# Kernel optimization log

Measured on AMD Instinct MI355X. Metric: run time of the kernel, lower is better.

## Reference

```python
import jax, jax.numpy as jnp
import numpy as np

B, S, D, E, R, TOP_K = 4, 4096, 2048, 6, 16, 2


def setup_inputs() -> dict:
    key = jax.random.key(0)
    ks = jax.random.split(key, 9)
    scale = 0.02
    return {
        "x": jax.random.normal(ks[0], (B, S, D), dtype=jnp.float32),
        "W_base": jax.random.normal(ks[1], (D, D), dtype=jnp.float32) * scale,
        "b_base": jax.random.normal(ks[2], (D,), dtype=jnp.float32) * scale,
        "A_s": jax.random.normal(ks[3], (D, R), dtype=jnp.float32) * scale,   # shared expert down-proj
        "B_s": jax.random.normal(ks[4], (R, D), dtype=jnp.float32) * scale,   # shared expert up-proj
        "A_r": jax.random.normal(ks[5], (E, D, R), dtype=jnp.float32) * scale,  # routed experts down-proj
        "B_r": jax.random.normal(ks[6], (E, R, D), dtype=jnp.float32) * scale,  # routed experts up-proj
        "W_router": jax.random.normal(ks[7], (D, E), dtype=jnp.float32) * scale,
        "b_router": jax.random.normal(ks[8], (E,), dtype=jnp.float32) * scale,
    }


def reference(x, W_base, b_base, A_s, B_s, A_r, B_r, W_router, b_router):
    # base_out computed under torch.no_grad() in the original -> stop_gradient
    base_out = jax.lax.stop_gradient(jnp.einsum("bsd,df->bsf", x, W_base) + b_base)

    # single shared LoRA expert (num_shared=1)
    shared_out = jnp.einsum("bsr,rf->bsf", jnp.einsum("bsd,dr->bsr", x, A_s), B_s)

    # router: softmax over experts, then top-k gating
    gates = jax.nn.softmax(jnp.einsum("bsd,de->bse", x, W_router) + b_router, axis=-1)
    topk_w, topk_i = jax.lax.top_k(gates, TOP_K)  # [B,S,K]
    # per-expert combine weight: sum of top-k weights scattered to expert slots
    w_per_e = jnp.sum(topk_w[..., None] * jax.nn.one_hot(topk_i, E, dtype=x.dtype), axis=2)  # [B,S,E]

    # routed LoRA experts: rank-16 down-proj per expert, weight in low-rank space,
    # then up-proj -- avoids materializing the [B,S,E,D] expert outputs.
    h = jnp.einsum("bsd,edr->bser", x, A_r)          # [B,S,E,R]
    hw = h * w_per_e[..., None]                       # fold gate weights into rank dim
    routed_out = jnp.einsum("bser,erf->bsf", hw, B_r)  # [B,S,D]

    return base_out + shared_out + routed_out
```

## Files before the change

kernel.cpp:

```cpp
#include <hip/hip_runtime.h>
#include <hip/hip_bf16.h>

typedef __hip_bfloat16 bf16;
typedef __attribute__((ext_vector_type(8))) __bf16 bf16x8;
typedef __attribute__((ext_vector_type(8))) short s16x8;
typedef __attribute__((ext_vector_type(4))) float f32x4;

#define AS1 __attribute__((address_space(1)))
#define AS3 __attribute__((address_space(3)))

#define DDIM 2048
#define KDIM 2176
#define TTOK 16384


__global__ __launch_bounds__(256) void prep_kernel(
    const float* __restrict__ W, const float* __restrict__ A_s,
    const float* __restrict__ A_r, const float* __restrict__ Bs,
    const float* __restrict__ Br, const float* __restrict__ Wr,
    bf16* __restrict__ Wcat, bf16* __restrict__ AcT, float* __restrict__ WrT) {
  __shared__ bf16 tl[64][65];
  int bid = blockIdx.x, tid = threadIdx.x;
  if (bid < 1024) {
    int bi = bid >> 5, bj = bid & 31;
    int k0 = bi * 64, n0 = bj * 64;
    int r = tid >> 2, c0 = (tid & 3) << 4;
#pragma unroll
    for (int q = 0; q < 4; ++q) {
      f32x4 v = *(const f32x4*)(W + (long)(k0 + r) * DDIM + n0 + c0 + q * 4);
#pragma unroll
      for (int j = 0; j < 4; ++j) tl[r][c0 + q * 4 + j] = __float2bfloat16(v[j]);
    }
    __syncthreads();
    __align__(16) bf16 o[16];
#pragma unroll
    for (int i = 0; i < 16; ++i) o[i] = tl[c0 + i][r];
    *(s16x8*)(Wcat + (long)(n0 + r) * KDIM + k0 + c0) = *(const s16x8*)o;
    *(s16x8*)(Wcat + (long)(n0 + r) * KDIM + k0 + c0 + 8) = *(const s16x8*)(o + 8);
  } else if (bid < 2048) {
    int idx = (bid - 1024) * 256 + tid;
    int c = idx >> 11, d = idx & 2047;
    float v = 0.f;
    if (c < 16)       v = A_s[d * 16 + c];
    else if (c < 112) { int cr = c - 16; v = A_r[((long)(cr >> 4) * DDIM + d) * 16 + (cr & 15)]; }
    AcT[(long)c * DDIM + d] = __float2bfloat16(v);
  } else if (bid < 3072) {
    int idx = (bid - 2048) * 256 + tid;
    int n = idx >> 7, c = idx & 127;
    float v = 0.f;
    if (c < 16)       v = Bs[c * DDIM + n];
    else if (c < 112) v = Br[(long)(c - 16) * DDIM + n];
    Wcat[(long)n * KDIM + 2048 + c] = __float2bfloat16(v);
  } else {
    int idx = (bid - 3072) * 256 + tid;
    int e = idx >> 11, d = idx & 2047;
    WrT[e * 2048 + d] = Wr[d * 6 + e];
  }
}


__global__ __launch_bounds__(256) void conv_router_kernel(
    const float* __restrict__ x, const float* __restrict__ WrT, const float* __restrict__ br,
    bf16* __restrict__ xh, float* __restrict__ gates) {
  int t = blockIdx.x;
  int tid = threadIdx.x;
  int d0 = tid * 8;
  f32x4 v0 = *(const f32x4*)(x + (long)t * DDIM + d0);
  f32x4 v1 = *(const f32x4*)(x + (long)t * DDIM + d0 + 4);
  __align__(16) bf16 tmp[8];
#pragma unroll
  for (int j = 0; j < 4; ++j) {
    tmp[j] = __float2bfloat16(v0[j]);
    tmp[4 + j] = __float2bfloat16(v1[j]);
  }
  *(s16x8*)(xh + (long)t * KDIM + d0) = *(const s16x8*)tmp;

  float p[6];
#pragma unroll
  for (int e = 0; e < 6; ++e) {
    f32x4 wa = *(const f32x4*)(WrT + e * 2048 + d0);
    f32x4 wb = *(const f32x4*)(WrT + e * 2048 + d0 + 4);
    float s = 0.f;
#pragma unroll
    for (int j = 0; j < 4; ++j) s += v0[j] * wa[j];
#pragma unroll
    for (int j = 0; j < 4; ++j) s += v1[j] * wb[j];
    p[e] = s;
  }
#pragma unroll
  for (int off = 32; off > 0; off >>= 1)
#pragma unroll
    for (int e = 0; e < 6; ++e) p[e] += __shfl_down(p[e], off);
  __shared__ float red[4][6];
  int wave = tid >> 6, lane = tid & 63;
  if (lane == 0)
#pragma unroll
    for (int e = 0; e < 6; ++e) red[wave][e] = p[e];
  __syncthreads();
  if (tid == 0) {
    float g[6], mx = -1e30f;
#pragma unroll
    for (int e = 0; e < 6; ++e) {
      g[e] = red[0][e] + red[1][e] + red[2][e] + red[3][e] + br[e];
      mx = fmaxf(mx, g[e]);
    }
    float s = 0.f;
#pragma unroll
    for (int e = 0; e < 6; ++e) { g[e] = __expf(g[e] - mx); s += g[e]; }
    float inv = 1.f / s;
#pragma unroll
    for (int e = 0; e < 6; ++e) g[e] *= inv;
    int i1 = 0; float w1 = g[0];
#pragma unroll
    for (int e = 1; e < 6; ++e) if (g[e] > w1) { w1 = g[e]; i1 = e; }
    int i2 = -1; float w2 = -1.f;
#pragma unroll
    for (int e = 0; e < 6; ++e) if (e != i1 && g[e] > w2) { w2 = g[e]; i2 = e; }
#pragma unroll
    for (int e = 0; e < 6; ++e)
      gates[(long)t * 6 + e] = (e == i1) ? w1 : (e == i2) ? w2 : 0.f;
  }
}


template <int ROWS>
__device__ __forceinline__ void stage_tile(const bf16* __restrict__ g, long rs,
                                           bf16* lds, int wave, int lane) {
#pragma unroll
  for (int i = 0; i < (ROWS >> 5); ++i) {
    int chunk_base = (i * 4 + wave) * 64;
    int byte = (chunk_base + lane) * 16;
    int row = byte >> 7;
    int col = (byte & 127) >> 1;
    __builtin_amdgcn_global_load_lds(
        (const AS1 void*)(g + (long)row * rs + col),
        (AS3 void*)(lds + chunk_base * 8), 16, 0, 0);
  }
}


__global__ __launch_bounds__(256) void lora_kernel(
    bf16* __restrict__ xh, const bf16* __restrict__ AcT,
    const float* __restrict__ gates) {
  __shared__ __align__(16) short smem[2 * 192 * 64];
  __shared__ float G[64][6];
  int tid = threadIdx.x, wave = tid >> 6, lane = tid & 63;
  long m0 = (long)blockIdx.x * 64;

  auto Xbuf = [&](int b) { return (bf16*)smem + b * 192 * 64; };
  auto Bbuf = [&](int b) { return (bf16*)smem + b * 192 * 64 + 64 * 64; };

  stage_tile<64>(xh + m0 * KDIM, KDIM, Xbuf(0), wave, lane);
  stage_tile<128>(AcT, DDIM, Bbuf(0), wave, lane);
  for (int i = tid; i < 384; i += 256) G[i / 6][i % 6] = gates[(m0 + i / 6) * 6 + i % 6];
  __syncthreads();

  f32x4 acc[7];
#pragma unroll
  for (int i = 0; i < 7; ++i) acc[i] = f32x4{0.f, 0.f, 0.f, 0.f};

  for (int kt = 0; kt < 32; ++kt) {
    int cur = kt & 1;
    if (kt < 31) {
      int k1 = (kt + 1) * 64;
      stage_tile<64>(xh + m0 * KDIM + k1, KDIM, Xbuf(cur ^ 1), wave, lane);
      stage_tile<128>(AcT + k1, DDIM, Bbuf(cur ^ 1), wave, lane);
    }
    if (kt > 0) {
      if (kt < 31) asm volatile("s_waitcnt vmcnt(6)" ::: "memory");
      else         asm volatile("s_waitcnt vmcnt(0)" ::: "memory");
      __builtin_amdgcn_sched_barrier(0);
      __builtin_amdgcn_s_barrier();
      __builtin_amdgcn_sched_barrier(0);
    }
    bf16* X_s = Xbuf(cur);
    bf16* B_s = Bbuf(cur);
#pragma unroll
    for (int kk = 0; kk < 2; ++kk) {
      bf16x8 a = *(const bf16x8*)(X_s + (16 * wave + (lane & 15)) * 64 + kk * 32 + (lane >> 4) * 8);
#pragma unroll
      for (int nr = 0; nr < 7; ++nr) {
        bf16x8 b = *(const bf16x8*)(B_s + (16 * nr + (lane & 15)) * 64 + kk * 32 + (lane >> 4) * 8);
        acc[nr] = __builtin_amdgcn_mfma_f32_16x16x32_bf16(a, b, acc[nr], 0, 0, 0);
      }
    }
    __builtin_amdgcn_sched_barrier(0);
    __builtin_amdgcn_s_barrier();
  }

  bf16* H = (bf16*)smem;
#pragma unroll
  for (int nr = 0; nr < 7; ++nr) {
    int c = nr * 16 + (lane & 15);
#pragma unroll
    for (int reg = 0; reg < 4; ++reg) {
      int tl = 16 * wave + 4 * (lane >> 4) + reg;
      float wgt = (c < 16) ? 1.f : G[tl][(c - 16) >> 4];
      H[tl * 128 + c] = __float2bfloat16(acc[nr][reg] * wgt);
    }
  }
  {
    int c = 112 + (lane & 15);
#pragma unroll
    for (int reg = 0; reg < 4; ++reg) {
      int tl = 16 * wave + 4 * (lane >> 4) + reg;
      H[tl * 128 + c] = __float2bfloat16(0.f);
    }
  }
  __syncthreads();
#pragma unroll
  for (int p = 0; p < 4; ++p) {
    int v = p * 256 + tid;
    int row = v >> 4, ch = (v & 15) * 8;
    *(s16x8*)(xh + (m0 + row) * KDIM + 2048 + ch) = *(const s16x8*)(H + row * 128 + ch);
  }
}


__global__ __launch_bounds__(512, 2) void gemm256_kernel(
    const bf16* __restrict__ xh, const bf16* __restrict__ Wcat,
    const float* __restrict__ b_base, float* __restrict__ out) {
  extern __shared__ char sm[];
  int tid = threadIdx.x, wave = tid >> 6, lane = tid & 63;
  int wr = wave >> 2, wc = wave & 3;

  int bid = blockIdx.x;
  int cpx = gridDim.x >> 3;
  int swz = (bid & 7) * cpx + (bid >> 3);
  long m0 = (long)(swz >> 3) * 256;
  int n0 = (swz & 7) * 256;

  int cp = ((lane >> 4) << 4) ^ (((lane >> 1) & 3) << 4);

  float bias[4];
#pragma unroll
  for (int nf = 0; nf < 4; ++nf) bias[nf] = b_base[n0 + wc * 64 + nf * 16 + (lane & 15)];

  f32x4 acc[8][4];
#pragma unroll
  for (int i = 0; i < 8; ++i)
#pragma unroll
    for (int j = 0; j < 4; ++j) acc[i][j] = f32x4{0.f, 0.f, 0.f, 0.f};

  const bf16* Agl = xh + m0 * KDIM;
  const bf16* Bgl = Wcat + (long)n0 * KDIM;

  auto stage_sub = [&](int t, int op, int h, int s) {
    int row = tid >> 2;
    int scol = ((((tid & 3) << 4) ^ (((row >> 1) & 3) << 4)) >> 1);
    const bf16* src = (op ? Bgl : Agl) + (long)(h * 128 + row) * KDIM + t * 64 + s * 32 + scol;
    char* dst = sm + (t & 1) * 65536 + op * 32768 + (h * 2 + s) * 8192 + tid * 16;
    __builtin_amdgcn_global_load_lds((const AS1 void*)src, (AS3 void*)dst, 16, 0, 0);
  };

  bf16x8 a[4], b[4];

  auto phase = [&](int buf, int ks, int mh, bool doStage, int stT, int stOp, int stKs, int vm) {
    if (mh == 0) {
      char* Bb = sm + buf * 65536 + 32768 + ((wc >> 1) * 2 + ks) * 8192;
#pragma unroll
      for (int n = 0; n < 4; ++n)
        b[n] = *(const bf16x8*)(Bb + ((wc & 1) * 64 + n * 16 + (lane & 15)) * 64 + cp);
    }
    char* Ab = sm + buf * 65536 + (wr * 2 + ks) * 8192;
#pragma unroll
    for (int j = 0; j < 4; ++j)
      a[j] = *(const bf16x8*)(Ab + ((mh * 4 + j) * 16 + (lane & 15)) * 64 + cp);
    if (doStage) { stage_sub(stT, stOp, 0, stKs); stage_sub(stT, stOp, 1, stKs); }
    __builtin_amdgcn_s_barrier();
    __builtin_amdgcn_s_setprio(1);
#pragma unroll
    for (int j = 0; j < 4; ++j)
#pragma unroll
      for (int n = 0; n < 4; ++n)
        acc[mh * 4 + j][n] = __builtin_amdgcn_mfma_f32_16x16x32_bf16(a[j], b[n], acc[mh * 4 + j][n], 0, 0, 0);
    __builtin_amdgcn_s_setprio(0);
    if (vm == 6)      asm volatile("s_waitcnt vmcnt(6)" ::: "memory");
    else if (vm == 4) asm volatile("s_waitcnt vmcnt(4)" ::: "memory");
    else if (vm == 0) asm volatile("s_waitcnt vmcnt(0)" ::: "memory");
    __builtin_amdgcn_s_barrier();
  };

  stage_sub(0, 0, 0, 0); stage_sub(0, 0, 1, 0); stage_sub(0, 1, 0, 0); stage_sub(0, 1, 1, 0);
  stage_sub(0, 0, 0, 1); stage_sub(0, 0, 1, 1); stage_sub(0, 1, 0, 1); stage_sub(0, 1, 1, 1);
  stage_sub(1, 0, 0, 0); stage_sub(1, 0, 1, 0); stage_sub(1, 1, 0, 0); stage_sub(1, 1, 1, 0);
  asm volatile("s_waitcnt vmcnt(8)" ::: "memory");
  __builtin_amdgcn_s_barrier();

  for (int i = 0; i < 16; ++i) {
    int t0 = 2 * i;
    phase(0, 0, 0, true, t0 + 1, 0, 1, -1);
    phase(0, 0, 1, true, t0 + 1, 1, 1, 6);
    phase(0, 1, 0, true, t0 + 2, 0, 0, -1);
    phase(0, 1, 1, true, t0 + 2, 1, 0, 6);
    phase(1, 0, 0, true, t0 + 2, 0, 1, -1);
    phase(1, 0, 1, true, t0 + 2, 1, 1, 6);
    phase(1, 1, 0, true, t0 + 3, 0, 0, -1);
    phase(1, 1, 1, true, t0 + 3, 1, 0, 6);
  }
  phase(0, 0, 0, true, 33, 0, 1, -1);
  phase(0, 0, 1, true, 33, 1, 1, 6);
  phase(0, 1, 0, false, 0, 0, 0, -1);
  phase(0, 1, 1, false, 0, 0, 0, 0);
  phase(1, 0, 0, false, 0, 0, 0, -1);
  phase(1, 0, 1, false, 0, 0, 0, -1);
  phase(1, 1, 0, false, 0, 0, 0, -1);
  phase(1, 1, 1, false, 0, 0, 0, -1);

  float* Cs = (float*)sm;
#pragma unroll
  for (int p = 0; p < 2; ++p) {
    __syncthreads();
#pragma unroll
    for (int q = 0; q < 4; ++q) {
#pragma unroll
      for (int nf = 0; nf < 4; ++nf) {
#pragma unroll
        for (int reg = 0; reg < 4; ++reg) {
          int r = wr * 64 + q * 16 + 4 * (lane >> 4) + reg;
          int colb = ((wc * 64 + nf * 16 + (lane & 15)) * 4) ^ (((r >> 2) & 3) << 6);
          *(float*)((char*)Cs + r * 1024 + colb) = acc[p * 4 + q][nf][reg] + bias[nf];
        }
      }
    }
    __syncthreads();
#pragma unroll 4
    for (int it = 0; it < 16; ++it) {
      int v = it * 512 + tid;
      int r = v >> 6, slot = v & 63;
      f32x4 val = *(const f32x4*)((char*)Cs + r * 1024 + ((slot << 4) ^ (((r >> 2) & 3) << 6)));
      long grow = m0 + (r >> 6) * 128 + p * 64 + (r & 63);
      *(f32x4*)(out + grow * DDIM + n0 + slot * 4) = val;
    }
  }
}


extern "C" void kernel_launch(void* const* d_in, const int* in_sizes, int n_in,
                              void* d_out, int out_size, void* d_ws, size_t ws_size,
                              hipStream_t stream) {
  const float* x        = (const float*)d_in[0];
  const float* W_base   = (const float*)d_in[1];
  const float* b_base   = (const float*)d_in[2];
  const float* A_s      = (const float*)d_in[3];
  const float* B_s      = (const float*)d_in[4];
  const float* A_r      = (const float*)d_in[5];
  const float* B_r      = (const float*)d_in[6];
  const float* W_router = (const float*)d_in[7];
  const float* b_router = (const float*)d_in[8];
  float* out = (float*)d_out;

  char* ws = (char*)d_ws;
  bf16*  xh    = (bf16*)(ws);
  bf16*  Wcat  = (bf16*)(ws + 71303168);
  bf16*  AcT   = (bf16*)(ws + 80216064);
  float* gates = (float*)(ws + 80740352);
  float* WrT   = (float*)(ws + 81133568);

  (void)hipFuncSetAttribute((const void*)gemm256_kernel,
                            hipFuncAttributeMaxDynamicSharedMemorySize, 131072);

  prep_kernel<<<3120, 256, 0, stream>>>(W_base, A_s, A_r, B_s, B_r, W_router, Wcat, AcT, WrT);
  conv_router_kernel<<<TTOK, 256, 0, stream>>>(x, WrT, b_router, xh, gates);
  lora_kernel<<<256, 256, 0, stream>>>(xh, AcT, gates);
  gemm256_kernel<<<512, 512, 131072, stream>>>(xh, Wcat, b_base, out);
}
```

Baseline: 267.3 us.

## Switch GEMM to 32x32x16 MFMA tiles and store results directly to global

Replaces the 16x16x32 bf16 MFMA tiling with 32x32x16 instructions. This halves the number of LDS fragment loads per MFMA and changes the register fragment layout to 4x2 tiles of 16 floats. The epilogue drops the LDS-staged, vectorized, coalesced write-out and instead writes each accumulator element straight to global memory. That removes the epilogue barriers and LDS traffic, but the global stores become scalar and strided by row, which may cost more store bandwidth.

```diff
diff --git a/kernel.cpp b/kernel.cpp
--- a/kernel.cpp
+++ b/kernel.cpp
@@ -5,6 +5,7 @@
 typedef __attribute__((ext_vector_type(8))) __bf16 bf16x8;
 typedef __attribute__((ext_vector_type(8))) short s16x8;
 typedef __attribute__((ext_vector_type(4))) float f32x4;
+typedef __attribute__((ext_vector_type(16))) float f32x16;
 
 #define AS1 __attribute__((address_space(1)))
 #define AS3 __attribute__((address_space(3)))
@@ -230,17 +231,17 @@
   long m0 = (long)(swz >> 3) * 256;
   int n0 = (swz & 7) * 256;
 
-  int cp = ((lane >> 4) << 4) ^ (((lane >> 1) & 3) << 4);
-
-  float bias[4];
-#pragma unroll
-  for (int nf = 0; nf < 4; ++nf) bias[nf] = b_base[n0 + wc * 64 + nf * 16 + (lane & 15)];
-
-  f32x4 acc[8][4];
-#pragma unroll
-  for (int i = 0; i < 8; ++i)
-#pragma unroll
-    for (int j = 0; j < 4; ++j) acc[i][j] = f32x4{0.f, 0.f, 0.f, 0.f};
+  float bias[2];
+#pragma unroll
+  for (int nf = 0; nf < 2; ++nf) bias[nf] = b_base[n0 + wc * 64 + nf * 32 + (lane & 31)];
+
+  f32x16 acc[4][2];
+#pragma unroll
+  for (int i = 0; i < 4; ++i)
+#pragma unroll
+    for (int j = 0; j < 2; ++j)
+#pragma unroll
+      for (int r = 0; r < 16; ++r) acc[i][j][r] = 0.f;
 
   const bf16* Agl = xh + m0 * KDIM;
   const bf16* Bgl = Wcat + (long)n0 * KDIM;
@@ -253,27 +254,40 @@
     __builtin_amdgcn_global_load_lds((const AS1 void*)src, (AS3 void*)dst, 16, 0, 0);
   };
 
-  bf16x8 a[4], b[4];
-
-  auto phase = [&](int buf, int ks, int mh, bool doStage, int stT, int stOp, int stKs, int vm) {
+  bf16x8 a[2][2], b[2][2];
+
+  auto phase = [&](int buf, int s, int mh, bool doStage, int stT, int stOp, int stKs, int vm) {
     if (mh == 0) {
-      char* Bb = sm + buf * 65536 + 32768 + ((wc >> 1) * 2 + ks) * 8192;
-#pragma unroll
-      for (int n = 0; n < 4; ++n)
-        b[n] = *(const bf16x8*)(Bb + ((wc & 1) * 64 + n * 16 + (lane & 15)) * 64 + cp);
-    }
-    char* Ab = sm + buf * 65536 + (wr * 2 + ks) * 8192;
-#pragma unroll
-    for (int j = 0; j < 4; ++j)
-      a[j] = *(const bf16x8*)(Ab + ((mh * 4 + j) * 16 + (lane & 15)) * 64 + cp);
+      char* Bb = sm + buf * 65536 + 32768 + ((wc >> 1) * 2 + s) * 8192;
+#pragma unroll
+      for (int nf = 0; nf < 2; ++nf) {
+        int r = (wc & 1) * 64 + nf * 32 + (lane & 31);
+#pragma unroll
+        for (int ks = 0; ks < 2; ++ks)
+          b[ks][nf] = *(const bf16x8*)(Bb + r * 64 +
+                        ((ks * 32 + ((lane >> 5) << 4)) ^ (((r >> 1) & 3) << 4)));
+      }
+    }
+    char* Ab = sm + buf * 65536 + (wr * 2 + s) * 8192;
+#pragma unroll
+    for (int mfl = 0; mfl < 2; ++mfl) {
+      int r = (mh * 2 + mfl) * 32 + (lane & 31);
+#pragma unroll
+      for (int ks = 0; ks < 2; ++ks)
+        a[ks][mfl] = *(const bf16x8*)(Ab + r * 64 +
+                      ((ks * 32 + ((lane >> 5) << 4)) ^ (((r >> 1) & 3) << 4)));
+    }
     if (doStage) { stage_sub(stT, stOp, 0, stKs); stage_sub(stT, stOp, 1, stKs); }
     __builtin_amdgcn_s_barrier();
     __builtin_amdgcn_s_setprio(1);
 #pragma unroll
-    for (int j = 0; j < 4; ++j)
-#pragma unroll
-      for (int n = 0; n < 4; ++n)
-        acc[mh * 4 + j][n] = __builtin_amdgcn_mfma_f32_16x16x32_bf16(a[j], b[n], acc[mh * 4 + j][n], 0, 0, 0);
+    for (int ks = 0; ks < 2; ++ks)
+#pragma unroll
+      for (int mfl = 0; mfl < 2; ++mfl)
+#pragma unroll
+        for (int nf = 0; nf < 2; ++nf)
+          acc[mh * 2 + mfl][nf] = __builtin_amdgcn_mfma_f32_32x32x16_bf16(
+              a[ks][mfl], b[ks][nf], acc[mh * 2 + mfl][nf], 0, 0, 0);
     __builtin_amdgcn_s_setprio(0);
     if (vm == 6)      asm volatile("s_waitcnt vmcnt(6)" ::: "memory");
     else if (vm == 4) asm volatile("s_waitcnt vmcnt(4)" ::: "memory");
@@ -307,32 +321,18 @@
   phase(1, 1, 0, false, 0, 0, 0, -1);
   phase(1, 1, 1, false, 0, 0, 0, -1);
 
-  float* Cs = (float*)sm;
-#pragma unroll
-  for (int p = 0; p < 2; ++p) {
-    __syncthreads();
-#pragma unroll
-    for (int q = 0; q < 4; ++q) {
-#pragma unroll
-      for (int nf = 0; nf < 4; ++nf) {
-#pragma unroll
-        for (int reg = 0; reg < 4; ++reg) {
-          int r = wr * 64 + q * 16 + 4 * (lane >> 4) + reg;
-          int colb = ((wc * 64 + nf * 16 + (lane & 15)) * 4) ^ (((r >> 2) & 3) << 6);
-          *(float*)((char*)Cs + r * 1024 + colb) = acc[p * 4 + q][nf][reg] + bias[nf];
-        }
+#pragma unroll
+  for (int mf = 0; mf < 4; ++mf)
+#pragma unroll
+    for (int nf = 0; nf < 2; ++nf) {
+      long gc = n0 + wc * 64 + nf * 32 + (lane & 31);
+#pragma unroll
+      for (int reg = 0; reg < 16; ++reg) {
+        int row = (reg & 3) + 8 * (reg >> 2) + 4 * (lane >> 5);
+        long gr = m0 + wr * 128 + mf * 32 + row;
+        out[gr * DDIM + gc] = acc[mf][nf][reg] + bias[nf];
       }
     }
-    __syncthreads();
-#pragma unroll 4
-    for (int it = 0; it < 16; ++it) {
-      int v = it * 512 + tid;
-      int r = v >> 6, slot = v & 63;
-      f32x4 val = *(const f32x4*)((char*)Cs + r * 1024 + ((slot << 4) ^ (((r >> 2) & 3) << 6)));
-      long grow = m0 + (r >> 6) * 128 + p * 64 + (r & 63);
-      *(f32x4*)(out + grow * DDIM + n0 + slot * 4) = val;
-    }
-  }
 }
 
 
```

Result: slower. 280.4 us (+4.9%).
